# Optimization experiments

Hardware: AMD Instinct MI355X
Metric: run time of the kernel (lower is better)

## Reference

```python
import math
import jax, jax.numpy as jnp
import numpy as np

B, S, D, H = 2, 2048, 1024, 16
DH = D // H


def setup_inputs() -> dict:
    key = jax.random.key(0)
    ks = jax.random.split(key, 6)
    scale = 1.0 / math.sqrt(D)  # xavier-ish scale for stability
    inp = {
        "query": jax.random.normal(ks[0], (B, S, D), jnp.float32),
        "mask": jax.random.randint(ks[1], (B, S, S), 0, 2) > 0,
        "Wq": jax.random.normal(ks[2], (D, D), jnp.float32) * scale,
        "bq": jnp.zeros((D,), jnp.float32),
        "Wk": jax.random.normal(ks[3], (D, D), jnp.float32) * scale,
        "bk": jnp.zeros((D,), jnp.float32),
        "Wv": jax.random.normal(ks[4], (D, D), jnp.float32) * scale,
        "bv": jnp.zeros((D,), jnp.float32),
        "Wo": jax.random.normal(ks[5], (D, D), jnp.float32) * scale,
        "bo": jnp.zeros((D,), jnp.float32),
    }
    return inp


def reference(query, mask, Wq, bq, Wk, bk, Wv, bv, Wo, bo):
    # self-attention: memory = query
    def shape(x):  # [B,S,D] -> [B,H,S,DH]
        return x.reshape(B, S, H, DH).transpose(0, 2, 1, 3)

    q = shape(query @ Wq.T + bq) / math.sqrt(DH)
    k = shape(query @ Wk.T + bk)
    v = shape(query @ Wv.T + bv)
    scores = jnp.einsum("bhqd,bhkd->bhqk", q, k)
    scores = jnp.where(mask[:, None, :, :], jnp.float32(-1e18), scores)
    attn = jax.nn.softmax(scores, axis=-1)
    # dropout is identity in eval mode
    ctx = jnp.einsum("bhqk,bhkd->bhqd", attn, v)
    ctx = ctx.transpose(0, 2, 1, 3).reshape(B, S, D)
    return ctx @ Wo.T + bo
```

## Files before the change

### kernel.cpp

```cpp
#include <hip/hip_runtime.h>

#define B_ 2
#define S_ 2048
#define D_ 1024
#define H_ 16
#define DH_ 64

typedef float f32x4 __attribute__((ext_vector_type(4)));
typedef short s16x8 __attribute__((ext_vector_type(8)));
typedef __bf16 bf16x8 __attribute__((ext_vector_type(8)));
typedef unsigned int uint;

template <typename T>
static __device__ auto mfma_sel(T a, T b, f32x4 c, int)
    -> decltype(__builtin_amdgcn_mfma_f32_16x16x32_bf16(a, b, c, 0, 0, 0)) {
  return __builtin_amdgcn_mfma_f32_16x16x32_bf16(a, b, c, 0, 0, 0);
}
template <typename T>
static __device__ f32x4 mfma_sel(T a, T b, f32x4 c, long) {
  return __builtin_amdgcn_mfma_f32_16x16x32_bf16(
      __builtin_bit_cast(bf16x8, a), __builtin_bit_cast(bf16x8, b), c, 0, 0, 0);
}
static __device__ __forceinline__ f32x4 mfma_bf16(s16x8 a, s16x8 b, f32x4 c) {
  return mfma_sel(a, b, c, 0);
}

static __device__ __forceinline__ short f2bf(float f) {
  unsigned u = __float_as_uint(f);
  u += 0x7fffu + ((u >> 16) & 1u);
  return (short)(u >> 16);
}

static __device__ __forceinline__ short f2bf_rn(float f) {
  return __builtin_bit_cast(short, (__bf16)f);
}

static __device__ __forceinline__ void async16(const short* g, short* l) {
  __builtin_amdgcn_global_load_lds(
      (const __attribute__((address_space(1))) unsigned int*)g,
      (__attribute__((address_space(3))) unsigned int*)l, 16, 0, 0);
}

__global__ void detect_mask_kernel(const uint* __restrict__ m,
                                   int* __restrict__ flag) {
  int lane = threadIdx.x;
  bool gt1 = false, notf = false;
  for (int i = 0; i < 16; ++i) {
    uint v = m[lane * 16 + i];
    if (v > 1u) gt1 = true;
    if (v != 0u && v != 0x3F800000u) notf = true;
  }
  unsigned long long b1 = __ballot(gt1);
  unsigned long long b2 = __ballot(notf);
  if (lane == 0) {
    int f;
    if (b1 == 0ull) f = 1;
    else if (b2 == 0ull) f = 2;
    else f = 0;
    *flag = f;
  }
}

__global__ __launch_bounds__(256) void build_bitmask_kernel(
    const void* __restrict__ mask, const int* __restrict__ flag,
    uint* __restrict__ bmT) {
  int w = blockIdx.x * 256 + threadIdx.x;
  int b = w >> 17;
  int rem = w & 131071;
  int q = rem >> 6;
  int kt = rem & 63;
  int mty = *flag;
  uint bits = 0;
  if (mty == 0) {
    const uint* p = (const uint*)((const unsigned char*)mask +
                                  ((size_t)b * S_ + q) * S_ + (size_t)kt * 32);
#pragma unroll
    for (int i = 0; i < 8; ++i) {
      uint v = p[i];
#pragma unroll
      for (int j = 0; j < 4; ++j)
        if ((v >> (8 * j)) & 0xffu) bits |= 1u << (i * 4 + j);
    }
  } else {
    const uint* p = (const uint*)mask + ((size_t)b * S_ + q) * S_ + kt * 32;
#pragma unroll
    for (int i = 0; i < 32; ++i)
      if (p[i]) bits |= 1u << i;
  }
  bmT[((size_t)b * (S_ / 32) + kt) * S_ + q] = bits;
}

__global__ __launch_bounds__(256) void convert_kernel(
    const float* __restrict__ q, const float* __restrict__ wq,
    const float* __restrict__ wk, const float* __restrict__ wv,
    short* __restrict__ qbf, short* __restrict__ wqkv) {
  int bid = blockIdx.x;
  int t = threadIdx.x;
  const float* src;
  short* dst;
  int rowbase, seg;
  if (bid < 2048)      { src = q;  dst = qbf;  rowbase = bid * 2;          seg = -1; }
  else if (bid < 2560) { src = wq; dst = wqkv; rowbase = (bid - 2048) * 2; seg = 0; }
  else if (bid < 3072) { src = wk; dst = wqkv; rowbase = (bid - 2560) * 2; seg = 1; }
  else                 { src = wv; dst = wqkv; rowbase = (bid - 3072) * 2; seg = 2; }
  int rl = rowbase + (t >> 7);
  int k = (t & 127) * 8;
  const float* s8 = src + (size_t)rl * 1024 + k;
  f32x4 a = *(const f32x4*)s8;
  f32x4 b = *(const f32x4*)(s8 + 4);
  s16x8 r;
  r[0] = f2bf(a[0]); r[1] = f2bf(a[1]); r[2] = f2bf(a[2]); r[3] = f2bf(a[3]);
  r[4] = f2bf(b[0]); r[5] = f2bf(b[1]); r[6] = f2bf(b[2]); r[7] = f2bf(b[3]);
  int grow = (seg < 0) ? rl : (seg * 1024 + rl);
  size_t chunk = ((size_t)(grow >> 4) * 32 + (k >> 5)) * 64 +
                 ((k >> 3) & 3) * 16 + (grow & 15);
  *(s16x8*)(dst + chunk * 8) = r;
}

__global__ __launch_bounds__(256) void convert_wo_kernel(
    const float* __restrict__ wo, short* __restrict__ wob) {
  size_t i = ((size_t)blockIdx.x * 256 + threadIdx.x) * 8;
  f32x4 a = *(const f32x4*)(wo + i);
  f32x4 b = *(const f32x4*)(wo + i + 4);
  s16x8 r;
  r[0] = f2bf(a[0]); r[1] = f2bf(a[1]); r[2] = f2bf(a[2]); r[3] = f2bf(a[3]);
  r[4] = f2bf(b[0]); r[5] = f2bf(b[1]); r[6] = f2bf(b[2]); r[7] = f2bf(b[3]);
  *(s16x8*)(wob + i) = r;
}

__global__ __launch_bounds__(256) void gemm_qkv_kernel(
    const short* __restrict__ A, const short* __restrict__ Bt,
    const float* __restrict__ bq, const float* __restrict__ bk,
    const float* __restrict__ bv, short* __restrict__ q_ws,
    short* __restrict__ KF, short* __restrict__ VF) {
  __shared__ short lds[8192];
  const int tid = threadIdx.x;
  const int lane = tid & 63;
  const int wave = tid >> 6;
  const int l16 = lane & 15;
  const int quad = lane >> 4;
  const int mb0 = blockIdx.x * 8;
  const int nb0 = blockIdx.y * 8;
  const int m0 = blockIdx.x * 128 + (wave >> 1) * 64;
  const int n0 = blockIdx.y * 128 + (wave & 1) * 64;
  const int g = tid >> 6, c = tid & 63;

  f32x4 acc[4][4];
#pragma unroll
  for (int i = 0; i < 4; ++i)
#pragma unroll
    for (int j = 0; j < 4; ++j) acc[i][j] = (f32x4){0.f, 0.f, 0.f, 0.f};

  for (int kb = 0; kb < 32; ++kb) {
    async16(A + (((size_t)(mb0 + g) * 32 + kb) * 64 + c) * 8, lds + tid * 8);
    async16(A + (((size_t)(mb0 + g + 4) * 32 + kb) * 64 + c) * 8,
            lds + 2048 + tid * 8);
    async16(Bt + (((size_t)(nb0 + g) * 32 + kb) * 64 + c) * 8,
            lds + 4096 + tid * 8);
    async16(Bt + (((size_t)(nb0 + g + 4) * 32 + kb) * 64 + c) * 8,
            lds + 6144 + tid * 8);
    __syncthreads();
    s16x8 a[4], b[4];
#pragma unroll
    for (int i = 0; i < 4; ++i)
      a[i] = *(const s16x8*)(lds + (((wave >> 1) * 4 + i) * 64 + lane) * 8);
#pragma unroll
    for (int j = 0; j < 4; ++j)
      b[j] = *(const s16x8*)(lds + 4096 + (((wave & 1) * 4 + j) * 64 + lane) * 8);
#pragma unroll
    for (int i = 0; i < 4; ++i)
#pragma unroll
      for (int j = 0; j < 4; ++j) acc[i][j] = mfma_bf16(a[i], b[j], acc[i][j]);
    __syncthreads();
  }

#pragma unroll
  for (int i = 0; i < 4; ++i) {
#pragma unroll
    for (int j = 0; j < 4; ++j) {
#pragma unroll
      for (int r = 0; r < 4; ++r) {
        int m = m0 + i * 16 + quad * 4 + r;
        int n = n0 + j * 16 + l16;
        int seg = n >> 10, nl = n & 1023;
        float bias = (seg == 0) ? bq[nl] : ((seg == 1) ? bk[nl] : bv[nl]);
        float v = acc[i][j][r] + bias;
        if (seg == 0) v *= 0.18033688011112042f;
        int bb = m >> 11, s = m & (S_ - 1);
        int hh = nl >> 6, dh = nl & 63;
        int bh = bb * H_ + hh;
        short bv16 = f2bf(v);
        if (seg == 0) {
          q_ws[((size_t)bh * S_ + s) * DH_ + dh] = bv16;
        } else if (seg == 1) {
          int kt = s >> 5, r5 = s & 31;
          int kkb = r5 >> 4, kl16 = r5 & 15;
          int kf = dh >> 5, qd = (dh >> 3) & 3, e = dh & 7;
          KF[(size_t)bh * 131072 +
             ((size_t)kt * 256 + (kkb * 2 + kf) * 64 + qd * 16 + kl16) * 8 + e] = bv16;
        } else {
          int kt = s >> 5, ko = s & 31;
          int hi = ko >> 4, qd = (ko >> 2) & 3, j4 = ko & 3;
          int nb = dh >> 4, vl16 = dh & 15, e = hi * 4 + j4;
          VF[(size_t)bh * 131072 +
             ((size_t)kt * 256 + nb * 64 + qd * 16 + vl16) * 8 + e] = bv16;
        }
      }
    }
  }
}

__global__ void attn_kernel(
    const short* __restrict__ Q, const short* __restrict__ KF,
    const short* __restrict__ VF, const uint* __restrict__ bmT,
    short* __restrict__ ctx_out) {
  __shared__ short lds[16384];
  const int tid = threadIdx.x;
  const int lane = tid & 63;
  const int wave = tid >> 6;
  const int l16 = lane & 15;
  const int quad = lane >> 4;
  const int xcd = blockIdx.x & 7;
  const int slot = blockIdx.x >> 3;
  const int bh = xcd * 4 + (slot >> 5);
  const int qt64 = slot & 31;
  const int b = bh >> 4;
  const int h = bh & 15;
  const int qbase = qt64 * 64 + wave * 16;
  const int qcol = qbase + l16;

  const short* Qh = Q + (size_t)bh * S_ * DH_;
  const short* KFb = KF + (size_t)bh * 131072;
  const short* VFb = VF + (size_t)bh * 131072;
  const uint* bmb = bmT + (size_t)b * (S_ / 32) * S_;

  s16x8 qf[2];
#pragma unroll
  for (int kf = 0; kf < 2; ++kf)
    qf[kf] = *(const s16x8*)(Qh + (size_t)qcol * DH_ + kf * 32 + quad * 8);

  f32x4 ctx[4];
#pragma unroll
  for (int nb = 0; nb < 4; ++nb) ctx[nb] = (f32x4){0.f, 0.f, 0.f, 0.f};
  float ls = 0.f;

  async16(KFb + tid * 8, lds + tid * 8);
  async16(KFb + 2048 + tid * 8, lds + 2048 + tid * 8);
  async16(VFb + tid * 8, lds + 4096 + tid * 8);
  async16(VFb + 2048 + tid * 8, lds + 6144 + tid * 8);
  uint w0 = bmb[qcol];
  uint w1 = bmb[(size_t)S_ + qcol];
  __syncthreads();

  for (int kt2 = 0; kt2 < S_ / 64; ++kt2) {
    uint wn0 = 0, wn1 = 0;
    if (kt2 < S_ / 64 - 1) {
      const int st = ((kt2 & 1) ^ 1) << 13;
      const short* kg = KFb + (size_t)(kt2 + 1) * 4096;
      const short* vg = VFb + (size_t)(kt2 + 1) * 4096;
      async16(kg + tid * 8, lds + st + tid * 8);
      async16(kg + 2048 + tid * 8, lds + st + 2048 + tid * 8);
      async16(vg + tid * 8, lds + st + 4096 + tid * 8);
      async16(vg + 2048 + tid * 8, lds + st + 6144 + tid * 8);
      wn0 = bmb[(size_t)(2 * kt2 + 2) * S_ + qcol];
      wn1 = bmb[(size_t)(2 * kt2 + 3) * S_ + qcol];
    }
    const short* kls = lds + ((kt2 & 1) << 13);
    const short* vls = kls + 4096;
    const uint wcur[2] = {w0 >> (quad * 4), w1 >> (quad * 4)};

#pragma unroll
    for (int kbt = 0; kbt < 2; ++kbt) {
      s16x8 ka[2][2];
#pragma unroll
      for (int kb = 0; kb < 2; ++kb)
#pragma unroll
        for (int kf = 0; kf < 2; ++kf)
          ka[kb][kf] =
              *(const s16x8*)(kls + kbt * 2048 + ((kb * 2 + kf) * 64 + lane) * 8);

      f32x4 sc[2];
#pragma unroll
      for (int kb = 0; kb < 2; ++kb) {
        f32x4 t = mfma_bf16(ka[kb][0], qf[0], (f32x4){0.f, 0.f, 0.f, 0.f});
        sc[kb] = mfma_bf16(ka[kb][1], qf[1], t);
      }

      s16x8 pa;
      float sum = 0.f;
#pragma unroll
      for (int kb = 0; kb < 2; ++kb)
#pragma unroll
        for (int r = 0; r < 4; ++r) {
          int bit = (wcur[kbt] >> (kb * 16 + r)) & 1;
          float p = bit ? 0.f : __builtin_amdgcn_exp2f(sc[kb][r]);
          sum += p;
          pa[kb * 4 + r] = f2bf_rn(p);
        }
      ls += sum;

#pragma unroll
      for (int nb = 0; nb < 4; ++nb) {
        s16x8 vb = *(const s16x8*)(vls + kbt * 2048 + (nb * 64 + lane) * 8);
        ctx[nb] = mfma_bf16(pa, vb, ctx[nb]);
      }
    }
    __syncthreads();
    w0 = wn0;
    w1 = wn1;
  }

  ls += __shfl_xor(ls, 16);
  ls += __shfl_xor(ls, 32);

#pragma unroll
  for (int r = 0; r < 4; ++r) {
    float lr = __shfl(ls, quad * 4 + r);
    float inv = 1.f / lr;
    int srow = qbase + quad * 4 + r;
#pragma unroll
    for (int nb = 0; nb < 4; ++nb) {
      int col = h * DH_ + nb * 16 + l16;
      ctx_out[(size_t)(b * S_ + srow) * D_ + col] = f2bf(ctx[nb][r] * inv);
    }
  }
}

__global__ __launch_bounds__(256) void gemm_final_kernel(
    const short* __restrict__ A, const short* __restrict__ Bt,
    const float* __restrict__ bias, float* __restrict__ out) {
  __shared__ short lds[8192];
  const int tid = threadIdx.x;
  const int lane = tid & 63;
  const int wave = tid >> 6;
  const int l16 = lane & 15;
  const int quad = lane >> 4;
  const int m0 = blockIdx.x * 128;
  const int n0 = blockIdx.y * 128;
  const int g = tid >> 6, c = tid & 63;
  const int r15 = c & 15, qd = c >> 4;

  f32x4 acc[4][4];
#pragma unroll
  for (int i = 0; i < 4; ++i)
#pragma unroll
    for (int j = 0; j < 4; ++j) acc[i][j] = (f32x4){0.f, 0.f, 0.f, 0.f};

  for (int k0 = 0; k0 < 1024; k0 += 32) {
    async16(A + (size_t)(m0 + g * 16 + r15) * 1024 + k0 + qd * 8, lds + tid * 8);
    async16(A + (size_t)(m0 + (g + 4) * 16 + r15) * 1024 + k0 + qd * 8,
            lds + 2048 + tid * 8);
    async16(Bt + (size_t)(n0 + g * 16 + r15) * 1024 + k0 + qd * 8,
            lds + 4096 + tid * 8);
    async16(Bt + (size_t)(n0 + (g + 4) * 16 + r15) * 1024 + k0 + qd * 8,
            lds + 6144 + tid * 8);
    __syncthreads();
    s16x8 a[4], b[4];
#pragma unroll
    for (int i = 0; i < 4; ++i)
      a[i] = *(const s16x8*)(lds + (((wave >> 1) * 4 + i) * 64 + lane) * 8);
#pragma unroll
    for (int j = 0; j < 4; ++j)
      b[j] = *(const s16x8*)(lds + 4096 + (((wave & 1) * 4 + j) * 64 + lane) * 8);
#pragma unroll
    for (int i = 0; i < 4; ++i)
#pragma unroll
      for (int j = 0; j < 4; ++j) acc[i][j] = mfma_bf16(a[i], b[j], acc[i][j]);
    __syncthreads();
  }

  const int mw = m0 + (wave >> 1) * 64;
  const int nw = n0 + (wave & 1) * 64;
#pragma unroll
  for (int i = 0; i < 4; ++i)
#pragma unroll
    for (int j = 0; j < 4; ++j)
#pragma unroll
      for (int r = 0; r < 4; ++r) {
        int m = mw + i * 16 + quad * 4 + r;
        int n = nw + j * 16 + l16;
        out[(size_t)m * 1024 + n] = acc[i][j][r] + bias[n];
      }
}

extern "C" void kernel_launch(void* const* d_in, const int* in_sizes, int n_in,
                              void* d_out, int out_size, void* d_ws,
                              size_t ws_size, hipStream_t stream) {
  const float* query = (const float*)d_in[0];
  const void* mask = d_in[1];
  const float* Wq = (const float*)d_in[2];
  const float* bq = (const float*)d_in[3];
  const float* Wk = (const float*)d_in[4];
  const float* bk = (const float*)d_in[5];
  const float* Wv = (const float*)d_in[6];
  const float* bv = (const float*)d_in[7];
  const float* Wo = (const float*)d_in[8];
  const float* bo = (const float*)d_in[9];

  const size_t NE = (size_t)B_ * S_ * D_;
  short* ws_s = (short*)d_ws;
  short* q_ws = ws_s;
  short* KF = ws_s + NE;
  short* VF = ws_s + 2 * NE;
  short* ctx_ws = ws_s + 3 * NE;
  short* wo_bf = ws_s;
  short* qbf = (short*)d_out;
  short* wqkv = qbf + NE;
  uint* bmT = (uint*)(wqkv + 3145728);
  int* flag = (int*)(bmT + 262144);

  detect_mask_kernel<<<1, 64, 0, stream>>>((const uint*)mask, flag);
  build_bitmask_kernel<<<1024, 256, 0, stream>>>(mask, flag, bmT);
  convert_kernel<<<3584, 256, 0, stream>>>(query, Wq, Wk, Wv, qbf, wqkv);

  gemm_qkv_kernel<<<dim3(32, 24), 256, 0, stream>>>(qbf, wqkv, bq, bk, bv,
                                                    q_ws, KF, VF);

  attn_kernel<<<1024, 256, 0, stream>>>(q_ws, KF, VF, bmT, ctx_ws);

  convert_wo_kernel<<<512, 256, 0, stream>>>(Wo, wo_bf);

  gemm_final_kernel<<<dim3(32, 8), 256, 0, stream>>>(ctx_ws, wo_bf, bo,
                                                     (float*)d_out);
}
```

Baseline: 249.9 us.

## Split attention key tiles across wave pairs with 128-query blocks and LDS reduction

The attention kernel now uses 512-thread blocks covering 128 queries. Each wave handles 32 queries, and the two waves of a pair split each 64-key tile, so every K/V fragment loaded from LDS serves two query groups. Partial context and row sums are combined through LDS at the end. The aim is to halve the number of blocks and the global-to-LDS K/V traffic per query, and to reuse each V fragment across two MFMAs. The cost is higher register pressure, an extra reduction pass with a barrier at the end, and fewer blocks in flight.

New measurement: 237.1 us. 5.1% less time.

```diff
diff --git a/kernel.cpp b/kernel.cpp
--- a/kernel.cpp
+++ b/kernel.cpp
@@ -210,46 +210,50 @@
   }
 }
 
-__global__ void attn_kernel(
+__global__ __launch_bounds__(512, 4) void attn_kernel(
     const short* __restrict__ Q, const short* __restrict__ KF,
     const short* __restrict__ VF, const uint* __restrict__ bmT,
     short* __restrict__ ctx_out) {
-  __shared__ short lds[16384];
+  __shared__ short lds[18432];
   const int tid = threadIdx.x;
   const int lane = tid & 63;
   const int wave = tid >> 6;
+  const int qw = wave >> 1;
+  const int kbt = wave & 1;
   const int l16 = lane & 15;
   const int quad = lane >> 4;
   const int xcd = blockIdx.x & 7;
   const int slot = blockIdx.x >> 3;
-  const int bh = xcd * 4 + (slot >> 5);
-  const int qt64 = slot & 31;
+  const int bh = xcd * 4 + (slot >> 4);
+  const int qt128 = slot & 15;
   const int b = bh >> 4;
   const int h = bh & 15;
-  const int qbase = qt64 * 64 + wave * 16;
-  const int qcol = qbase + l16;
+  const int qbase = qt128 * 128 + qw * 32;
 
   const short* Qh = Q + (size_t)bh * S_ * DH_;
   const short* KFb = KF + (size_t)bh * 131072;
   const short* VFb = VF + (size_t)bh * 131072;
   const uint* bmb = bmT + (size_t)b * (S_ / 32) * S_;
 
-  s16x8 qf[2];
-#pragma unroll
-  for (int kf = 0; kf < 2; ++kf)
-    qf[kf] = *(const s16x8*)(Qh + (size_t)qcol * DH_ + kf * 32 + quad * 8);
-
-  f32x4 ctx[4];
-#pragma unroll
-  for (int nb = 0; nb < 4; ++nb) ctx[nb] = (f32x4){0.f, 0.f, 0.f, 0.f};
-  float ls = 0.f;
+  s16x8 qf[2][2];
+#pragma unroll
+  for (int qg = 0; qg < 2; ++qg)
+#pragma unroll
+    for (int kf = 0; kf < 2; ++kf)
+      qf[qg][kf] = *(const s16x8*)(Qh + (size_t)(qbase + qg * 16 + l16) * DH_ +
+                                   kf * 32 + quad * 8);
+
+  f32x4 ctx[2][4];
+#pragma unroll
+  for (int qg = 0; qg < 2; ++qg)
+#pragma unroll
+    for (int nb = 0; nb < 4; ++nb) ctx[qg][nb] = (f32x4){0.f, 0.f, 0.f, 0.f};
+  float ls[2] = {0.f, 0.f};
 
   async16(KFb + tid * 8, lds + tid * 8);
-  async16(KFb + 2048 + tid * 8, lds + 2048 + tid * 8);
   async16(VFb + tid * 8, lds + 4096 + tid * 8);
-  async16(VFb + 2048 + tid * 8, lds + 6144 + tid * 8);
-  uint w0 = bmb[qcol];
-  uint w1 = bmb[(size_t)S_ + qcol];
+  uint w0 = bmb[(size_t)kbt * S_ + qbase + l16];
+  uint w1 = bmb[(size_t)kbt * S_ + qbase + 16 + l16];
   __syncthreads();
 
   for (int kt2 = 0; kt2 < S_ / 64; ++kt2) {
@@ -259,70 +263,96 @@
       const short* kg = KFb + (size_t)(kt2 + 1) * 4096;
       const short* vg = VFb + (size_t)(kt2 + 1) * 4096;
       async16(kg + tid * 8, lds + st + tid * 8);
-      async16(kg + 2048 + tid * 8, lds + st + 2048 + tid * 8);
       async16(vg + tid * 8, lds + st + 4096 + tid * 8);
-      async16(vg + 2048 + tid * 8, lds + st + 6144 + tid * 8);
-      wn0 = bmb[(size_t)(2 * kt2 + 2) * S_ + qcol];
-      wn1 = bmb[(size_t)(2 * kt2 + 3) * S_ + qcol];
+      wn0 = bmb[(size_t)(2 * (kt2 + 1) + kbt) * S_ + qbase + l16];
+      wn1 = bmb[(size_t)(2 * (kt2 + 1) + kbt) * S_ + qbase + 16 + l16];
     }
     const short* kls = lds + ((kt2 & 1) << 13);
     const short* vls = kls + 4096;
-    const uint wcur[2] = {w0 >> (quad * 4), w1 >> (quad * 4)};
-
-#pragma unroll
-    for (int kbt = 0; kbt < 2; ++kbt) {
-      s16x8 ka[2][2];
+
+    s16x8 ka[2][2];
+#pragma unroll
+    for (int kb = 0; kb < 2; ++kb)
+#pragma unroll
+      for (int kf = 0; kf < 2; ++kf)
+        ka[kb][kf] =
+            *(const s16x8*)(kls + kbt * 2048 + ((kb * 2 + kf) * 64 + lane) * 8);
+
+    s16x8 pa[2];
+    const uint wsh[2] = {w0 >> (quad * 4), w1 >> (quad * 4)};
+#pragma unroll
+    for (int qg = 0; qg < 2; ++qg) {
+      f32x4 sc[2];
+#pragma unroll
+      for (int kb = 0; kb < 2; ++kb) {
+        f32x4 t = mfma_bf16(ka[kb][0], qf[qg][0], (f32x4){0.f, 0.f, 0.f, 0.f});
+        sc[kb] = mfma_bf16(ka[kb][1], qf[qg][1], t);
+      }
+      float sum = 0.f;
 #pragma unroll
       for (int kb = 0; kb < 2; ++kb)
 #pragma unroll
-        for (int kf = 0; kf < 2; ++kf)
-          ka[kb][kf] =
-              *(const s16x8*)(kls + kbt * 2048 + ((kb * 2 + kf) * 64 + lane) * 8);
-
-      f32x4 sc[2];
-#pragma unroll
-      for (int kb = 0; kb < 2; ++kb) {
-        f32x4 t = mfma_bf16(ka[kb][0], qf[0], (f32x4){0.f, 0.f, 0.f, 0.f});
-        sc[kb] = mfma_bf16(ka[kb][1], qf[1], t);
-      }
-
-      s16x8 pa;
-      float sum = 0.f;
-#pragma unroll
-      for (int kb = 0; kb < 2; ++kb)
-#pragma unroll
         for (int r = 0; r < 4; ++r) {
-          int bit = (wcur[kbt] >> (kb * 16 + r)) & 1;
+          int bit = (wsh[qg] >> (kb * 16 + r)) & 1;
           float p = bit ? 0.f : __builtin_amdgcn_exp2f(sc[kb][r]);
           sum += p;
-          pa[kb * 4 + r] = f2bf_rn(p);
+          pa[qg][kb * 4 + r] = f2bf_rn(p);
         }
-      ls += sum;
-
-#pragma unroll
-      for (int nb = 0; nb < 4; ++nb) {
-        s16x8 vb = *(const s16x8*)(vls + kbt * 2048 + (nb * 64 + lane) * 8);
-        ctx[nb] = mfma_bf16(pa, vb, ctx[nb]);
-      }
+      ls[qg] += sum;
+    }
+
+#pragma unroll
+    for (int nb = 0; nb < 4; ++nb) {
+      s16x8 vb = *(const s16x8*)(vls + kbt * 2048 + (nb * 64 + lane) * 8);
+#pragma unroll
+      for (int qg = 0; qg < 2; ++qg)
+        ctx[qg][nb] = mfma_bf16(pa[qg], vb, ctx[qg][nb]);
     }
     __syncthreads();
     w0 = wn0;
     w1 = wn1;
   }
 
-  ls += __shfl_xor(ls, 16);
-  ls += __shfl_xor(ls, 32);
-
-#pragma unroll
-  for (int r = 0; r < 4; ++r) {
-    float lr = __shfl(ls, quad * 4 + r);
-    float inv = 1.f / lr;
-    int srow = qbase + quad * 4 + r;
-#pragma unroll
-    for (int nb = 0; nb < 4; ++nb) {
-      int col = h * DH_ + nb * 16 + l16;
-      ctx_out[(size_t)(b * S_ + srow) * D_ + col] = f2bf(ctx[nb][r] * inv);
-    }
+  float* fl = (float*)lds;
+  const int foff = qw * 2176;
+  if (kbt) {
+#pragma unroll
+    for (int qg = 0; qg < 2; ++qg) {
+#pragma unroll
+      for (int nb = 0; nb < 4; ++nb)
+#pragma unroll
+        for (int r = 0; r < 4; ++r)
+          fl[foff + ((qg * 4 + nb) * 4 + r) * 64 + lane] = ctx[qg][nb][r];
+      fl[foff + 2048 + qg * 64 + lane] = ls[qg];
+    }
+  }
+  __syncthreads();
+  if (!kbt) {
+#pragma unroll
+    for (int qg = 0; qg < 2; ++qg) {
+#pragma unroll
+      for (int nb = 0; nb < 4; ++nb)
+#pragma unroll
+        for (int r = 0; r < 4; ++r)
+          ctx[qg][nb][r] += fl[foff + ((qg * 4 + nb) * 4 + r) * 64 + lane];
+      ls[qg] += fl[foff + 2048 + qg * 64 + lane];
+      ls[qg] += __shfl_xor(ls[qg], 16);
+      ls[qg] += __shfl_xor(ls[qg], 32);
+    }
+
+#pragma unroll
+    for (int qg = 0; qg < 2; ++qg)
+#pragma unroll
+      for (int r = 0; r < 4; ++r) {
+        float lr = __shfl(ls[qg], quad * 4 + r);
+        float inv = 1.f / lr;
+        int srow = qbase + qg * 16 + quad * 4 + r;
+#pragma unroll
+        for (int nb = 0; nb < 4; ++nb) {
+          int col = h * DH_ + nb * 16 + l16;
+          ctx_out[(size_t)(b * S_ + srow) * D_ + col] = f2bf(ctx[qg][nb][r] * inv);
+        }
+      }
   }
 }
 
@@ -416,7 +446,7 @@
   gemm_qkv_kernel<<<dim3(32, 24), 256, 0, stream>>>(qbf, wqkv, bq, bk, bv,
                                                     q_ws, KF, VF);
 
-  attn_kernel<<<1024, 256, 0, stream>>>(q_ws, KF, VF, bmT, ctx_ws);
+  attn_kernel<<<512, 512, 0, stream>>>(q_ws, KF, VF, bmT, ctx_ws);
 
   convert_wo_kernel<<<512, 256, 0, stream>>>(Wo, wo_bf);
 
```
